# Kernel tuning notes

Measured on AMD Instinct MI355X. Metric: run time of the kernel, lower is better.

## Reference

```python
import jax, jax.numpy as jnp
import numpy as np

D_MODEL = 256
GAMMA = 0.9          # ret_D is built in the torch forward but never applied to the output; kept for fidelity notes
SCALE_BASE = 512     # XPOS default
TEMP = 10000.0
TWO_PI = 2.0 * np.pi


def sine_pos_embed(x):
    """DETR-style 1D sine position embedding with an all-ones mask (as in forward).
    x: [B,T,C] -> pos: [1,T,C] (mask is [1,T] ones, so batch dim broadcasts)."""
    T, C = x.shape[1], x.shape[2]
    x_embed = jnp.arange(1, T + 1, dtype=jnp.float32)          # cumsum of ones
    x_embed = x_embed / (x_embed[-1] + 1e-6) * TWO_PI          # normalize=True
    dim_t = TEMP ** (2.0 * (jnp.arange(C) // 2).astype(jnp.float32) / C)
    pos = x_embed[:, None] / dim_t                             # [T,C]
    pos = jnp.stack([jnp.sin(pos[:, 0::2]), jnp.cos(pos[:, 1::2])], axis=2).reshape(T, C)
    return pos[None].astype(x.dtype)


def _dup_interleave(m):
    # [L, d/2] -> [L, d], columns repeated pairwise: [a,b] -> [a,a,b,b]
    return jnp.repeat(m, 2, axis=-1)


def _rotate_every_two(x):
    x1, x2 = x[..., 0::2], x[..., 1::2]
    return jnp.stack([-x2, x1], axis=-1).reshape(x.shape)


def xpos_apply(x, downscale=False):
    """RetNet XPOS rotary embedding. x: [B,L,d]."""
    L, d = x.shape[1], x.shape[2]
    half = d // 2
    scale_vec = (jnp.arange(0, d, 2, dtype=jnp.float32) + 0.4 * d) / (1.4 * d)   # [d/2]
    power = jnp.arange(L, dtype=jnp.float32) / SCALE_BASE
    scale = scale_vec[None, :] ** power[:, None]                                  # [L, d/2]
    inv_freq = 1.0 / (TEMP ** (jnp.arange(half, dtype=jnp.float32) / half))
    sinusoid = jnp.arange(L, dtype=jnp.float32)[:, None] * inv_freq[None, :]      # [L, d/2]
    sin, cos = jnp.sin(sinusoid), jnp.cos(sinusoid)
    if downscale:
        scale = 1.0 / scale
    sin_s = _dup_interleave(sin * scale)[None].astype(x.dtype)   # [1,L,d]
    cos_s = _dup_interleave(cos * scale)[None].astype(x.dtype)
    return x * cos_s + _rotate_every_two(x) * sin_s


def setup_inputs() -> dict:
    key = jax.random.key(0)
    ks = jax.random.split(key, 8)
    B, TXT, VID, D = 16, 32, 2048, D_MODEL
    S = TXT + VID
    inp = {
        "src": jax.random.normal(ks[0], (B, S, D), dtype=jnp.float32),
        "learn_vid_ret": jax.random.normal(ks[1], (VID * VID, 1), dtype=jnp.float32),
        "W_txt_Q": jax.random.normal(ks[2], (D, D), dtype=jnp.float32) / D,
        "W_txt_K": jax.random.normal(ks[3], (D, D), dtype=jnp.float32) / D,
        "W_txt_V": jax.random.normal(ks[4], (D, D), dtype=jnp.float32) / D,
        "W_vid_Q": jax.random.normal(ks[5], (D, D), dtype=jnp.float32) / D,
        "W_vid_K": jax.random.normal(ks[6], (D, D), dtype=jnp.float32) / D,
        "W_vid_V": jax.random.normal(ks[7], (D, D), dtype=jnp.float32) / D,
        "txt_length": TXT,
    }
    return inp


def reference(src, learn_vid_ret, W_txt_Q, W_txt_K, W_txt_V, W_vid_Q, W_vid_K, W_vid_V, txt_length):
    S = src.shape[1]
    vid_length = S - txt_length

    # learned retention mask over the video block
    learn_ret = jax.nn.sigmoid(learn_vid_ret.reshape(vid_length, vid_length))
    diag = jnp.eye(vid_length, dtype=src.dtype)
    video_ret = (1.0 - diag) * learn_ret
    loss_sparsity = jnp.mean(jnp.abs(video_ret))

    # full [S,S] mask: ones everywhere, sigmoid(learned) on the vid-vid block
    ret_mask = jnp.ones((S, S), dtype=src.dtype).at[txt_length:, txt_length:].set(learn_ret)

    txt_mem = src[:, :txt_length]   # [B,TXT,D]
    vid_mem = src[:, txt_length:]   # [B,VID,D]

    pos = sine_pos_embed(txt_mem)   # [1,TXT,D]
    txt_Q = (pos + txt_mem) @ W_txt_Q
    txt_K = (pos + txt_mem) @ W_txt_K
    vid_Q = xpos_apply(vid_mem @ W_vid_Q)
    vid_K = xpos_apply(vid_mem @ W_vid_K, downscale=True)

    Q = jnp.concatenate([txt_Q, vid_Q], axis=1)                  # [B,S,D]
    K = jnp.concatenate([txt_K, vid_K], axis=1)                  # [B,S,D]
    V = jnp.concatenate([txt_mem @ W_txt_V, vid_mem @ W_vid_V], axis=1)

    # retention: QK^T elementwise-masked (no softmax), then weighted V sum
    scores = jnp.einsum('bsd,btd->bst', Q, K) * ret_mask[None]   # [B,S,S]
    out = scores @ V                                             # [B,S,D]
    return out, loss_sparsity
```

## Files before the change

kernel.cpp:

```cpp
#include <hip/hip_runtime.h>

#define B_   16
#define TXT  32
#define VID  2048
#define D_   256
#define S_   2080
#define SP   2176
#define NKT  34
#define ITERS 33

typedef unsigned short ushort_t;
typedef __attribute__((ext_vector_type(8))) short short8;
typedef __attribute__((ext_vector_type(4))) short short4v;
typedef __attribute__((ext_vector_type(4))) float f32x4;
typedef __attribute__((ext_vector_type(16))) float f32x16;

__device__ __forceinline__ ushort_t f2bf(float f) {
  unsigned u = __builtin_bit_cast(unsigned, f);
  unsigned r = (u + 0x7FFFu + ((u >> 16) & 1u)) >> 16;
  return (ushort_t)r;
}
__device__ __forceinline__ float bf2f(ushort_t h) {
  unsigned u = ((unsigned)h) << 16;
  return __builtin_bit_cast(float, u);
}

__device__ __forceinline__ void g2l16(void* lds, const void* g) {
  __builtin_amdgcn_global_load_lds(
      (const __attribute__((address_space(1))) char*)g,
      (__attribute__((address_space(3))) char*)lds, 16, 0, 0);
}

__device__ __forceinline__ f32x4 mfma16(short8 a, short8 b, f32x4 c) {
  return __builtin_amdgcn_mfma_f32_16x16x32_bf16(a, b, c, 0, 0, 0);
}
__device__ __forceinline__ f32x16 mfma32(short8 a, short8 b, f32x16 c) {
  return __builtin_amdgcn_mfma_f32_32x32x16_bf16(a, b, c, 0, 0, 0);
}


__global__ void tbl_kernel(float* __restrict__ tbl) {
  int idx = blockIdx.x * 256 + threadIdx.x;
  int n = idx >> 7, i = idx & 127;
  float invf = powf(10000.0f, -(float)i / 128.0f);
  float ang = (float)n * invf;
  float s, co;
  sincosf(ang, &s, &co);
  float sv = ((float)(2 * i) + 102.4f) / 358.4f;
  float sc = powf(sv, (float)n / 512.0f);
  float4 r;
  r.x = co * sc; r.y = s * sc; r.z = co / sc; r.w = s / sc;
  *(float4*)(tbl + (size_t)idx * 4) = r;
}

__global__ void sig_loss_kernel(const float* __restrict__ learn, ushort_t* __restrict__ sigp,
                                float* __restrict__ loss) {
  const int tid = threadIdx.x;
  const int base = (blockIdx.x * 256 + tid) * 8;
  float4 v0 = *(const float4*)(learn + base);
  float4 v1 = *(const float4*)(learn + base + 4);
  float vals[8] = {v0.x, v0.y, v0.z, v0.w, v1.x, v1.y, v1.z, v1.w};
  float acc = 0.f;
  short8 sh;
  #pragma unroll
  for (int j = 0; j < 8; ++j) {
    int idx = base + j;
    float s = 1.0f / (1.0f + expf(-vals[j]));
    sh[j] = (short)f2bf(s);
    int rr = idx >> 11, cc = idx & 2047;
    if (rr != cc) acc += s;
  }
  *(short8*)(sigp + base) = sh;
  __shared__ float red[256];
  red[tid] = acc;
  __syncthreads();
  #pragma unroll
  for (int st = 128; st > 0; st >>= 1) {
    if (tid < st) red[tid] += red[tid + st];
    __syncthreads();
  }
  if (tid == 0) atomicAdd(loss, red[0] * (1.0f / 4194304.0f));
}

__global__ void wt_kernel(const float* __restrict__ Wq, const float* __restrict__ Wk,
                          const float* __restrict__ Wv, ushort_t* __restrict__ WT) {
  __shared__ float t[64][68];
  const int k0 = blockIdx.x * 64, n0 = blockIdx.y * 64, mt = blockIdx.z;
  const float* W = (mt == 0) ? Wq : (mt == 1) ? Wk : Wv;
  int tid = threadIdx.x;
  int r = tid >> 4, cq = (tid & 15) * 4;
  #pragma unroll
  for (int m = 0; m < 4; ++m) {
    int k = m * 16 + r;
    float4 v = *(const float4*)(W + (size_t)(k0 + k) * 256 + n0 + cq);
    t[k][cq] = v.x; t[k][cq + 1] = v.y; t[k][cq + 2] = v.z; t[k][cq + 3] = v.w;
  }
  __syncthreads();
  #pragma unroll
  for (int m = 0; m < 4; ++m) {
    int n = m * 16 + r;
    short4v h;
    h[0] = (short)f2bf(t[cq + 0][n]);
    h[1] = (short)f2bf(t[cq + 1][n]);
    h[2] = (short)f2bf(t[cq + 2][n]);
    h[3] = (short)f2bf(t[cq + 3][n]);
    *(short4v*)(WT + ((size_t)mt * D_ + n0 + n) * D_ + k0 + cq) = h;
  }
}

__global__ void txt_kernel(const float* __restrict__ src,
                           const float* __restrict__ Wq, const float* __restrict__ Wk,
                           const float* __restrict__ Wv,
                           ushort_t* __restrict__ Qp, ushort_t* __restrict__ Ks,
                           ushort_t* __restrict__ VTs) {
  __shared__ float a_s[8][256];
  __shared__ float x_s[8][256];
  const int tg = blockIdx.x;
  const int b  = blockIdx.y;
  const int c  = threadIdx.x;
  #pragma unroll
  for (int t = 0; t < 8; ++t) {
    int row = tg * 8 + t;
    float x = src[((size_t)b * S_ + row) * D_ + c];
    float xe = (float)(row + 1) * (6.283185307179586f / (32.0f + 1e-6f));
    int i = c >> 1;
    float dimt = powf(10000.0f, (2.0f * (float)i) / 256.0f);
    float ang = xe / dimt;
    float pv = (c & 1) ? cosf(ang) : sinf(ang);
    x_s[t][c] = x;
    a_s[t][c] = x + pv;
  }
  __syncthreads();
  float q[8] = {0,0,0,0,0,0,0,0}, k[8] = {0,0,0,0,0,0,0,0}, v[8] = {0,0,0,0,0,0,0,0};
  for (int kk = 0; kk < 256; ++kk) {
    float wq = Wq[(size_t)kk * 256 + c];
    float wk = Wk[(size_t)kk * 256 + c];
    float wv = Wv[(size_t)kk * 256 + c];
    #pragma unroll
    for (int t = 0; t < 8; ++t) {
      q[t] = fmaf(a_s[t][kk], wq, q[t]);
      k[t] = fmaf(a_s[t][kk], wk, k[t]);
      v[t] = fmaf(x_s[t][kk], wv, v[t]);
    }
  }
  #pragma unroll
  for (int t = 0; t < 8; ++t) {
    int row = tg * 8 + t;
    Qp[((size_t)b * SP + row) * D_ + c] = f2bf(q[t]);
    Ks[(((size_t)(b * NKT)) << 14) + (c >> 4) * 1024 + row * 16 + (c & 15)] = f2bf(k[t]);
    VTs[(((size_t)(b * NKT)) << 14) + (row >> 4) * 4096 + c * 16 + (row & 15)] = f2bf(v[t]);
  }
}

__global__ __launch_bounds__(256, 2) void vid_gemm(
    const float* __restrict__ src, const ushort_t* __restrict__ WT,
    const float* __restrict__ tbl,
    ushort_t* __restrict__ Qp, ushort_t* __restrict__ Ks, ushort_t* __restrict__ VTs) {
  __shared__ __align__(16) ushort_t ldsA[64 * 64];
  __shared__ __align__(16) ushort_t ldsB[64 * 64];

  const int rt = blockIdx.x;
  const int b  = blockIdx.y;
  const int ct = blockIdx.z;
  const int nt = ct >> 2;
  const int n0 = (ct & 3) * 64;
  const int tid = threadIdx.x;
  const int wv = tid >> 6, lane = tid & 63, l15 = lane & 15, l4 = lane >> 4;

  f32x4 acc[4];
  #pragma unroll
  for (int t2 = 0; t2 < 4; ++t2) { acc[t2][0] = 0.f; acc[t2][1] = 0.f; acc[t2][2] = 0.f; acc[t2][3] = 0.f; }

  for (int kk = 0; kk < 256; kk += 64) {
    #pragma unroll
    for (int m = 0; m < 4; ++m) {
      int q = m * 256 + tid;
      int r = q >> 4;
      int kc = (q & 15) * 4;
      const float4 v = *(const float4*)(src + ((size_t)b * S_ + TXT + rt * 64 + r) * D_ + kk + kc);
      short4v h;
      h[0] = (short)f2bf(v.x); h[1] = (short)f2bf(v.y);
      h[2] = (short)f2bf(v.z); h[3] = (short)f2bf(v.w);
      int off = ((r << 7) + (kc << 1)) ^ ((r & 7) << 4);
      *(short4v*)((char*)ldsA + off) = h;
    }
    #pragma unroll
    for (int m = 0; m < 2; ++m) {
      int p = (m * 256 + tid) * 16;
      int nl = p >> 7;
      int c = (p & 127) ^ ((nl & 7) << 4);
      g2l16((char*)ldsB + p, (const char*)(WT + ((size_t)nt * D_ + n0 + nl) * D_ + kk) + c);
    }
    __syncthreads();
    #pragma unroll
    for (int ks = 0; ks < 2; ++ks) {
      int ar = wv * 16 + l15;
      int aoff = ((ar << 7) + ((ks * 32 + l4 * 8) << 1)) ^ ((ar & 7) << 4);
      short8 av = *(const short8*)((const char*)ldsA + aoff);
      #pragma unroll
      for (int t2 = 0; t2 < 4; ++t2) {
        int nl = t2 * 16 + l15;
        int boff = ((nl << 7) + ((ks * 32 + l4 * 8) << 1)) ^ ((nl & 7) << 4);
        short8 bv = *(const short8*)((const char*)ldsB + boff);
        acc[t2] = mfma16(av, bv, acc[t2]);
      }
    }
    __syncthreads();
  }

  const int rowl = wv * 16 + l4 * 4;
  if (nt < 2) {
    #pragma unroll
    for (int t2 = 0; t2 < 4; ++t2) {
      int c = n0 + t2 * 16 + l15;
      #pragma unroll
      for (int r = 0; r < 4; ++r) {
        int n = rt * 64 + rowl + r;
        float x = acc[t2][r];
        float xp = __shfl_xor(x, 1);
        const float4 tb = *(const float4*)(tbl + ((size_t)n * 128 + (c >> 1)) * 4);
        float cs = (nt == 0) ? tb.x : tb.z;
        float ss = (nt == 0) ? tb.y : tb.w;
        float val = (c & 1) ? fmaf(x, cs, xp * ss) : fmaf(x, cs, -xp * ss);
        if (nt == 0) {
          Qp[((size_t)b * SP + TXT + n) * D_ + c] = f2bf(val);
        } else {
          int kvg = TXT + n;
          Ks[(((size_t)(b * NKT + (kvg >> 6))) << 14) + (c >> 4) * 1024 + (kvg & 63) * 16 + (c & 15)] = f2bf(val);
        }
      }
    }
  } else {
    #pragma unroll
    for (int t2 = 0; t2 < 4; ++t2)
      #pragma unroll
      for (int r = 0; r < 4; ++r) {
        int rr = rowl + r;
        int cc = t2 * 16 + l15;
        int off = ((rr << 7) + (cc << 1)) ^ ((rr & 7) << 4);
        *(ushort_t*)((char*)ldsA + off) = f2bf(acc[t2][r]);
      }
    __syncthreads();
    int n = tid >> 2;
    int rc = (tid & 3) * 16;
    short8 o0, o1;
    #pragma unroll
    for (int j = 0; j < 8; ++j) {
      int rr = rc + j;
      int off = ((rr << 7) + (n << 1)) ^ ((rr & 7) << 4);
      o0[j] = *(const short*)((const char*)ldsA + off);
    }
    #pragma unroll
    for (int j = 0; j < 8; ++j) {
      int rr = rc + 8 + j;
      int off = ((rr << 7) + (n << 1)) ^ ((rr & 7) << 4);
      o1[j] = *(const short*)((const char*)ldsA + off);
    }
    int d = n0 + n;
    int kvg0 = TXT + rt * 64 + rc;
    size_t base = (((size_t)(b * NKT + (kvg0 >> 6))) << 14) + ((kvg0 >> 4) & 3) * 4096 + d * 16;
    *(short8*)(VTs + base) = o0;
    *(short8*)(VTs + base + 8) = o1;
  }
}

__global__ __launch_bounds__(256, 2) void attn_kernel(
    const ushort_t* __restrict__ Qp, const ushort_t* __restrict__ Ks,
    const ushort_t* __restrict__ VTs, const ushort_t* __restrict__ sigp,
    float* __restrict__ out) {
  __shared__ __align__(16) ushort_t Kb[16384];
  __shared__ __align__(16) ushort_t Vb[16384];
  __shared__ __align__(16) ushort_t Pb[4096];

  const int flat = blockIdx.x;
  const int wg = (flat & 7) * 66 + (flat >> 3);
  const int b  = wg / ITERS;
  const int qt = wg % ITERS;
  const int tid = threadIdx.x;
  const int wid = tid >> 6, lane = tid & 63;
  const int l31 = lane & 31, l5 = lane >> 5;
  const int qh = wid >> 1, kh = wid & 1, d0 = wid * 64;
  const int q0 = qt * 64;

  short8 qf[16];
  {
    const ushort_t* qrow = Qp + ((size_t)b * SP + q0 + qh * 32 + l31) * D_ + l5 * 8;
    #pragma unroll
    for (int ks = 0; ks < 16; ++ks) qf[ks] = *(const short8*)(qrow + ks * 16);
  }

  f32x16 oacc[2][2];
  #pragma unroll
  for (int i = 0; i < 2; ++i)
    #pragma unroll
    for (int j = 0; j < 2; ++j)
      #pragma unroll
      for (int r = 0; r < 16; ++r) oacc[i][j][r] = 0.f;

  const char* ksrc = (const char*)Ks + (((size_t)(b * NKT)) << 15);
  const char* vsrc = (const char*)VTs + (((size_t)(b * NKT)) << 15);

  ushort_t mvu[16];
  auto ldmask = [&](int t) {
    unsigned ki = (unsigned)(t * 64 + kh * 32 + l31 - TXT);
    bool kok = ki < (unsigned)VID;
    #pragma unroll
    for (int r = 0; r < 16; ++r) {
      int qloc = qh * 32 + (r & 3) + 8 * (r >> 2) + 4 * l5;
      unsigned qi = (unsigned)(q0 + qloc - TXT);
      bool ok = kok && (qi < (unsigned)VID);
      mvu[r] = sigp[ok ? ((size_t)qi * VID + ki) : 0];
    }
  };

  #pragma unroll
  for (int m = 0; m < 8; ++m) { int s = m * 256 + tid; g2l16((char*)Kb + s * 16, ksrc + s * 16); }
  __builtin_amdgcn_sched_barrier(0);
  ldmask(0);
  __builtin_amdgcn_sched_barrier(0);
  #pragma unroll
  for (int m = 0; m < 8; ++m) { int s = m * 256 + tid; g2l16((char*)Vb + s * 16, vsrc + s * 16); }
  __builtin_amdgcn_sched_barrier(0);
  asm volatile("s_waitcnt vmcnt(24)" ::: "memory");
  __builtin_amdgcn_sched_barrier(0);
  __builtin_amdgcn_s_barrier();
  __builtin_amdgcn_sched_barrier(0);

  for (int kt = 0; kt < ITERS; ++kt) {
    f32x16 s0, s1;
    #pragma unroll
    for (int r = 0; r < 16; ++r) { s0[r] = 0.f; s1[r] = 0.f; }
    const int krow = (kh * 32 + l31) * 32 + l5 * 16;
    __builtin_amdgcn_s_setprio(1);
    #pragma unroll
    for (int ks = 0; ks < 8; ++ks) {
      short8 kfa = *(const short8*)((const char*)Kb + ks * 2048 + krow);
      short8 kfb = *(const short8*)((const char*)Kb + (ks + 8) * 2048 + krow);
      s0 = mfma32(qf[ks], kfa, s0);
      s1 = mfma32(qf[ks + 8], kfb, s1);
    }
    __builtin_amdgcn_s_setprio(0);

    {
      unsigned ki = (unsigned)(kt * 64 + kh * 32 + l31 - TXT);
      bool kok = ki < (unsigned)VID;
      const int kvl = kh * 32 + l31;
      const int ksp = kvl >> 4;
      #pragma unroll
      for (int r = 0; r < 16; ++r) {
        int qloc = qh * 32 + (r & 3) + 8 * (r >> 2) + 4 * l5;
        unsigned qi = (unsigned)(q0 + qloc - TXT);
        float mvf = (kok && qi < (unsigned)VID) ? bf2f(mvu[r]) : 1.0f;
        float sv = (s0[r] + s1[r]) * mvf;
        int off = (ksp * 2048 + qloc * 32 + (kvl & 15) * 2)
                  ^ ((((unsigned)qloc >> 2) & 3) << 5) ^ ((ksp & 1) << 6);
        *(ushort_t*)((char*)Pb + off) = f2bf(sv);
      }
    }

    asm volatile("s_waitcnt vmcnt(0) lgkmcnt(0)" ::: "memory");
    __builtin_amdgcn_sched_barrier(0);
    __builtin_amdgcn_s_barrier();
    __builtin_amdgcn_sched_barrier(0);

    {
      const char* src = ksrc + ((size_t)(kt + 1) << 15);
      #pragma unroll
      for (int m = 0; m < 8; ++m) { int s = m * 256 + tid; g2l16((char*)Kb + s * 16, src + s * 16); }
    }
    __builtin_amdgcn_sched_barrier(0);

    __builtin_amdgcn_s_setprio(1);
    #pragma unroll
    for (int ks = 0; ks < 4; ++ks) {
      int p0 = (ks * 2048 + l31 * 32 + l5 * 16) ^ ((((unsigned)l31 >> 2) & 3) << 5) ^ ((ks & 1) << 6);
      int p1 = (ks * 2048 + (32 + l31) * 32 + l5 * 16) ^ ((((unsigned)(32 + l31) >> 2) & 3) << 5) ^ ((ks & 1) << 6);
      short8 pf0 = *(const short8*)((const char*)Pb + p0);
      short8 pf1 = *(const short8*)((const char*)Pb + p1);
      short8 vf0 = *(const short8*)((const char*)Vb + ks * 8192 + (d0 + l31) * 32 + l5 * 16);
      short8 vf1 = *(const short8*)((const char*)Vb + ks * 8192 + (d0 + 32 + l31) * 32 + l5 * 16);
      oacc[0][0] = mfma32(pf0, vf0, oacc[0][0]);
      oacc[0][1] = mfma32(pf0, vf1, oacc[0][1]);
      oacc[1][0] = mfma32(pf1, vf0, oacc[1][0]);
      oacc[1][1] = mfma32(pf1, vf1, oacc[1][1]);
    }
    __builtin_amdgcn_s_setprio(0);
    __builtin_amdgcn_sched_barrier(0);
    __builtin_amdgcn_s_barrier();
    __builtin_amdgcn_sched_barrier(0);

    ldmask(kt + 1);
    __builtin_amdgcn_sched_barrier(0);
    {
      const char* src = vsrc + ((size_t)(kt + 1) << 15);
      #pragma unroll
      for (int m = 0; m < 8; ++m) { int s = m * 256 + tid; g2l16((char*)Vb + s * 16, src + s * 16); }
    }
    __builtin_amdgcn_sched_barrier(0);
    asm volatile("s_waitcnt vmcnt(24)" ::: "memory");
    __builtin_amdgcn_sched_barrier(0);
    __builtin_amdgcn_s_barrier();
    __builtin_amdgcn_sched_barrier(0);
  }

  #pragma unroll
  for (int qg2 = 0; qg2 < 2; ++qg2)
    #pragma unroll
    for (int dg = 0; dg < 2; ++dg)
      #pragma unroll
      for (int reg = 0; reg < 16; ++reg) {
        int qg = q0 + qg2 * 32 + (reg & 3) + 8 * (reg >> 2) + 4 * l5;
        int dd = d0 + dg * 32 + l31;
        if (qg < S_) out[((size_t)b * S_ + qg) * D_ + dd] = oacc[qg2][dg][reg];
      }
}

extern "C" void kernel_launch(void* const* d_in, const int* in_sizes, int n_in,
                              void* d_out, int out_size, void* d_ws, size_t ws_size,
                              hipStream_t stream) {
  (void)in_sizes; (void)n_in; (void)out_size; (void)ws_size;
  const float* src   = (const float*)d_in[0];
  const float* learn = (const float*)d_in[1];
  const float* Wtq = (const float*)d_in[2];
  const float* Wtk = (const float*)d_in[3];
  const float* Wtv = (const float*)d_in[4];
  const float* Wvq = (const float*)d_in[5];
  const float* Wvk = (const float*)d_in[6];
  const float* Wvv = (const float*)d_in[7];
  float* out = (float*)d_out;

  char* ws = (char*)d_ws;
  const size_t QKV_ONE = (size_t)B_ * SP * D_ * 2;
  const size_t QP_OFF  = 0;
  const size_t KS_OFF  = QP_OFF + QKV_ONE;
  const size_t VT_OFF  = KS_OFF + QKV_ONE;
  const size_t SIG_OFF = VT_OFF + QKV_ONE;
  const size_t TBL_OFF = SIG_OFF + (size_t)VID * VID * 2;
  const size_t WT_OFF  = TBL_OFF + (size_t)VID * 128 * 4 * sizeof(float);

  ushort_t* Qp   = (ushort_t*)(ws + QP_OFF);
  ushort_t* Ks   = (ushort_t*)(ws + KS_OFF);
  ushort_t* VTs  = (ushort_t*)(ws + VT_OFF);
  ushort_t* sigp = (ushort_t*)(ws + SIG_OFF);
  float*    tbl  = (float*)(ws + TBL_OFF);
  ushort_t* WT   = (ushort_t*)(ws + WT_OFF);

  float* loss = out + (size_t)B_ * S_ * D_;

  hipMemsetAsync(ws, 0, SIG_OFF, stream);
  hipMemsetAsync(loss, 0, sizeof(float), stream);

  tbl_kernel<<<1024, 256, 0, stream>>>(tbl);
  sig_loss_kernel<<<2048, 256, 0, stream>>>(learn, sigp, loss);
  wt_kernel<<<dim3(4, 4, 3), 256, 0, stream>>>(Wvq, Wvk, Wvv, WT);
  txt_kernel<<<dim3(4, B_), 256, 0, stream>>>(src, Wtq, Wtk, Wtv, Qp, Ks, VTs);
  vid_gemm<<<dim3(32, B_, 12), 256, 0, stream>>>(src, WT, tbl, Qp, Ks, VTs);
  attn_kernel<<<dim3(528), 256, 0, stream>>>(Qp, Ks, VTs, sigp, out);
}
```

Measured before the change: 339.9 us.

## Stream-K attention over flattened tile space with atomic output accumulation

Flattens the (batch, q-tile, kv-tile) iteration space and splits it evenly across 512 persistent blocks. This replaces the 528 whole-row blocks, which quantize badly against the CU count. Partial outputs are flushed with float atomics into a zeroed output buffer, and Q is reloaded whenever the tile changes. The score MFMA is transposed so the mask is read from a transposed sigmoid table, and P is packed with v_cvt_pk_bf16 into a new swizzled layout. A dedicated kernel now zeroes only the pad regions instead of memsetting the whole workspace. The costs are atomic traffic, extra Q reloads at tile boundaries, and nondeterministic summation order.

```diff
diff --git a/kernel.cpp b/kernel.cpp
--- a/kernel.cpp
+++ b/kernel.cpp
@@ -7,7 +7,7 @@
 #define S_   2080
 #define SP   2176
 #define NKT  34
-#define ITERS 33
+#define GTOT 17424
 
 typedef unsigned short ushort_t;
 typedef __attribute__((ext_vector_type(8))) short short8;
@@ -53,25 +53,29 @@
   *(float4*)(tbl + (size_t)idx * 4) = r;
 }
 
-__global__ void sig_loss_kernel(const float* __restrict__ learn, ushort_t* __restrict__ sigp,
-                                float* __restrict__ loss) {
+__global__ void sig_kernel(const float* __restrict__ learn, ushort_t* __restrict__ sigT,
+                           float* __restrict__ loss) {
+  __shared__ ushort_t t[64][68];
+  __shared__ float red[256];
+  const int bi = blockIdx.x;
+  const int bj = blockIdx.y;
   const int tid = threadIdx.x;
-  const int base = (blockIdx.x * 256 + tid) * 8;
-  float4 v0 = *(const float4*)(learn + base);
-  float4 v1 = *(const float4*)(learn + base + 4);
-  float vals[8] = {v0.x, v0.y, v0.z, v0.w, v1.x, v1.y, v1.z, v1.w};
+  const int r = tid >> 2, c0 = (tid & 3) * 16;
+  const int q = bi * 64 + r;
   float acc = 0.f;
-  short8 sh;
-  #pragma unroll
-  for (int j = 0; j < 8; ++j) {
-    int idx = base + j;
-    float s = 1.0f / (1.0f + expf(-vals[j]));
-    sh[j] = (short)f2bf(s);
-    int rr = idx >> 11, cc = idx & 2047;
-    if (rr != cc) acc += s;
-  }
-  *(short8*)(sigp + base) = sh;
-  __shared__ float red[256];
+  const float* row = learn + (size_t)q * VID + bj * 64 + c0;
+  #pragma unroll
+  for (int j4 = 0; j4 < 4; ++j4) {
+    float4 v = *(const float4*)(row + j4 * 4);
+    float vv[4] = {v.x, v.y, v.z, v.w};
+    #pragma unroll
+    for (int j = 0; j < 4; ++j) {
+      int kv = bj * 64 + c0 + j4 * 4 + j;
+      float s = 1.0f / (1.0f + expf(-vv[j]));
+      if (q != kv) acc += s;
+      t[r][c0 + j4 * 4 + j] = f2bf(s);
+    }
+  }
   red[tid] = acc;
   __syncthreads();
   #pragma unroll
@@ -80,6 +84,34 @@
     __syncthreads();
   }
   if (tid == 0) atomicAdd(loss, red[0] * (1.0f / 4194304.0f));
+  short8 o0, o1;
+  #pragma unroll
+  for (int j = 0; j < 8; ++j) o0[j] = (short)t[c0 + j][r];
+  #pragma unroll
+  for (int j = 0; j < 8; ++j) o1[j] = (short)t[c0 + 8 + j][r];
+  ushort_t* dst = sigT + (size_t)(bj * 64 + r) * VID + bi * 64 + c0;
+  *(short8*)dst = o0;
+  *(short8*)(dst + 8) = o1;
+}
+
+__global__ void pad0_kernel(ushort_t* __restrict__ Qp, ushort_t* __restrict__ Ks,
+                            ushort_t* __restrict__ VTs) {
+  int i = blockIdx.x * 256 + threadIdx.x;
+  short8 z = {0, 0, 0, 0, 0, 0, 0, 0};
+  if (i < 49152) {
+    int bb = i / 3072, rem = i - bb * 3072;
+    int row = 2080 + (rem >> 5), c8 = (rem & 31) * 8;
+    *(short8*)(Qp + ((size_t)bb * SP + row) * D_ + c8) = z;
+  } else if (i < 65536) {
+    int j = i - 49152; int bb = j >> 10; int rem = j & 1023;
+    int kstep = rem >> 6, ch = rem & 63;
+    size_t base = ((size_t)(bb * NKT + 32)) << 14;
+    *(short8*)(Ks + base + kstep * 1024 + 512 + ch * 8) = z;
+  } else if (i < 81920) {
+    int j = i - 65536; int bb = j >> 10; int rem = j & 1023;
+    size_t base = (((size_t)(bb * NKT + 32)) << 14) + 8192;
+    *(short8*)(VTs + base + rem * 8) = z;
+  }
 }
 
 __global__ void wt_kernel(const float* __restrict__ Wq, const float* __restrict__ Wk,
@@ -266,28 +298,53 @@
 
 __global__ __launch_bounds__(256, 2) void attn_kernel(
     const ushort_t* __restrict__ Qp, const ushort_t* __restrict__ Ks,
-    const ushort_t* __restrict__ VTs, const ushort_t* __restrict__ sigp,
+    const ushort_t* __restrict__ VTs, const ushort_t* __restrict__ sigT,
     float* __restrict__ out) {
   __shared__ __align__(16) ushort_t Kb[16384];
   __shared__ __align__(16) ushort_t Vb[16384];
   __shared__ __align__(16) ushort_t Pb[4096];
 
-  const int flat = blockIdx.x;
-  const int wg = (flat & 7) * 66 + (flat >> 3);
-  const int b  = wg / ITERS;
-  const int qt = wg % ITERS;
+  const int kblk = blockIdx.x;
+  const int bs = (kblk & 7) * 64 + (kblk >> 3);
+  int g = bs * 34 + (bs >> 5);
+  const int gend = (bs + 1) * 34 + ((bs + 1) >> 5);
+
   const int tid = threadIdx.x;
   const int wid = tid >> 6, lane = tid & 63;
   const int l31 = lane & 31, l5 = lane >> 5;
   const int qh = wid >> 1, kh = wid & 1, d0 = wid * 64;
-  const int q0 = qt * 64;
+
+  int b = g / 1089, rem = g - b * 1089, qt = rem / 33, kvt = rem - qt * 33;
 
   short8 qf[16];
-  {
-    const ushort_t* qrow = Qp + ((size_t)b * SP + q0 + qh * 32 + l31) * D_ + l5 * 8;
+  auto ldq = [&](int bb, int qq) {
+    const ushort_t* qrow = Qp + ((size_t)bb * SP + qq * 64 + qh * 32 + l31) * D_ + l5 * 8;
     #pragma unroll
     for (int ks = 0; ks < 16; ++ks) qf[ks] = *(const short8*)(qrow + ks * 16);
-  }
+  };
+
+  ushort_t mvu[16];
+  auto ldmask = [&](int qq, int tt) {
+    unsigned qi = (unsigned)(qq * 64 + qh * 32 + l31 - TXT);
+    bool qok = qi < (unsigned)VID;
+    #pragma unroll
+    for (int r = 0; r < 16; ++r) {
+      unsigned ki = (unsigned)(tt * 64 + kh * 32 + (r & 3) + 8 * (r >> 2) + 4 * l5 - TXT);
+      bool ok = qok && (ki < (unsigned)VID);
+      mvu[r] = sigT[ok ? ((size_t)ki * VID + qi) : 0];
+    }
+  };
+
+  auto stageK = [&](int bb, int tt) {
+    const char* src = (const char*)Ks + (((size_t)(bb * NKT + tt)) << 15);
+    #pragma unroll
+    for (int m = 0; m < 8; ++m) { int s = m * 256 + tid; g2l16((char*)Kb + s * 16, src + s * 16); }
+  };
+  auto stageV = [&](int bb, int tt) {
+    const char* src = (const char*)VTs + (((size_t)(bb * NKT + tt)) << 15);
+    #pragma unroll
+    for (int m = 0; m < 8; ++m) { int s = m * 256 + tid; g2l16((char*)Vb + s * 16, src + s * 16); }
+  };
 
   f32x16 oacc[2][2];
   #pragma unroll
@@ -297,64 +354,67 @@
       #pragma unroll
       for (int r = 0; r < 16; ++r) oacc[i][j][r] = 0.f;
 
-  const char* ksrc = (const char*)Ks + (((size_t)(b * NKT)) << 15);
-  const char* vsrc = (const char*)VTs + (((size_t)(b * NKT)) << 15);
-
-  ushort_t mvu[16];
-  auto ldmask = [&](int t) {
-    unsigned ki = (unsigned)(t * 64 + kh * 32 + l31 - TXT);
-    bool kok = ki < (unsigned)VID;
-    #pragma unroll
-    for (int r = 0; r < 16; ++r) {
-      int qloc = qh * 32 + (r & 3) + 8 * (r >> 2) + 4 * l5;
-      unsigned qi = (unsigned)(q0 + qloc - TXT);
-      bool ok = kok && (qi < (unsigned)VID);
-      mvu[r] = sigp[ok ? ((size_t)qi * VID + ki) : 0];
-    }
+  auto flushO = [&](int bb, int qq) {
+    #pragma unroll
+    for (int qg2 = 0; qg2 < 2; ++qg2)
+      #pragma unroll
+      for (int dg = 0; dg < 2; ++dg)
+        #pragma unroll
+        for (int r = 0; r < 16; ++r) {
+          int qg = qq * 64 + qg2 * 32 + (r & 3) + 8 * (r >> 2) + 4 * l5;
+          int dd = d0 + dg * 32 + l31;
+          if (qg < S_)
+            unsafeAtomicAdd(&out[((size_t)bb * S_ + qg) * D_ + dd], oacc[qg2][dg][r]);
+          oacc[qg2][dg][r] = 0.f;
+        }
   };
 
-  #pragma unroll
-  for (int m = 0; m < 8; ++m) { int s = m * 256 + tid; g2l16((char*)Kb + s * 16, ksrc + s * 16); }
-  __builtin_amdgcn_sched_barrier(0);
-  ldmask(0);
-  __builtin_amdgcn_sched_barrier(0);
-  #pragma unroll
-  for (int m = 0; m < 8; ++m) { int s = m * 256 + tid; g2l16((char*)Vb + s * 16, vsrc + s * 16); }
-  __builtin_amdgcn_sched_barrier(0);
-  asm volatile("s_waitcnt vmcnt(24)" ::: "memory");
+  stageK(b, kvt);
+  ldmask(qt, kvt);
+  stageV(b, kvt);
+  ldq(b, qt);
+  asm volatile("s_waitcnt vmcnt(0)" ::: "memory");
   __builtin_amdgcn_sched_barrier(0);
   __builtin_amdgcn_s_barrier();
   __builtin_amdgcn_sched_barrier(0);
 
-  for (int kt = 0; kt < ITERS; ++kt) {
+  while (g < gend) {
+    int gn = (g + 1 < GTOT) ? g + 1 : GTOT - 1;
+    int nb = gn / 1089, nrem = gn - nb * 1089, nqt = nrem / 33, nkvt = nrem - nqt * 33;
+
     f32x16 s0, s1;
     #pragma unroll
     for (int r = 0; r < 16; ++r) { s0[r] = 0.f; s1[r] = 0.f; }
-    const int krow = (kh * 32 + l31) * 32 + l5 * 16;
+    const int arow = (kh * 32 + l31) * 32 + l5 * 16;
     __builtin_amdgcn_s_setprio(1);
     #pragma unroll
     for (int ks = 0; ks < 8; ++ks) {
-      short8 kfa = *(const short8*)((const char*)Kb + ks * 2048 + krow);
-      short8 kfb = *(const short8*)((const char*)Kb + (ks + 8) * 2048 + krow);
-      s0 = mfma32(qf[ks], kfa, s0);
-      s1 = mfma32(qf[ks + 8], kfb, s1);
+      short8 ka = *(const short8*)((const char*)Kb + ks * 2048 + arow);
+      short8 kc = *(const short8*)((const char*)Kb + (ks + 8) * 2048 + arow);
+      s0 = mfma32(ka, qf[ks], s0);
+      s1 = mfma32(kc, qf[ks + 8], s1);
     }
     __builtin_amdgcn_s_setprio(0);
 
     {
-      unsigned ki = (unsigned)(kt * 64 + kh * 32 + l31 - TXT);
-      bool kok = ki < (unsigned)VID;
-      const int kvl = kh * 32 + l31;
-      const int ksp = kvl >> 4;
+      unsigned qi = (unsigned)(qt * 64 + qh * 32 + l31 - TXT);
+      bool qok = qi < (unsigned)VID;
+      const int prow = qh * 32 + l31;
       #pragma unroll
-      for (int r = 0; r < 16; ++r) {
-        int qloc = qh * 32 + (r & 3) + 8 * (r >> 2) + 4 * l5;
-        unsigned qi = (unsigned)(q0 + qloc - TXT);
-        float mvf = (kok && qi < (unsigned)VID) ? bf2f(mvu[r]) : 1.0f;
-        float sv = (s0[r] + s1[r]) * mvf;
-        int off = (ksp * 2048 + qloc * 32 + (kvl & 15) * 2)
-                  ^ ((((unsigned)qloc >> 2) & 3) << 5) ^ ((ksp & 1) << 6);
-        *(ushort_t*)((char*)Pb + off) = f2bf(sv);
+      for (int t = 0; t < 4; ++t) {
+        float p[4];
+        #pragma unroll
+        for (int j = 0; j < 4; ++j) {
+          int r = t * 4 + j;
+          unsigned ki = (unsigned)(kvt * 64 + kh * 32 + j + 8 * t + 4 * l5 - TXT);
+          float mvf = (qok && ki < (unsigned)VID) ? bf2f(mvu[r]) : 1.0f;
+          p[j] = (s0[r] + s1[r]) * mvf;
+        }
+        unsigned w0, w1;
+        asm("v_cvt_pk_bf16_f32 %0, %1, %2" : "=v"(w0) : "v"(p[0]), "v"(p[1]));
+        asm("v_cvt_pk_bf16_f32 %0, %1, %2" : "=v"(w1) : "v"(p[2]), "v"(p[3]));
+        int off = (prow * 128 + kh * 64 + t * 16 + l5 * 8) ^ ((l31 & 7) << 4);
+        *(uint2*)((char*)Pb + off) = make_uint2(w0, w1);
       }
     }
 
@@ -363,18 +423,14 @@
     __builtin_amdgcn_s_barrier();
     __builtin_amdgcn_sched_barrier(0);
 
-    {
-      const char* src = ksrc + ((size_t)(kt + 1) << 15);
-      #pragma unroll
-      for (int m = 0; m < 8; ++m) { int s = m * 256 + tid; g2l16((char*)Kb + s * 16, src + s * 16); }
-    }
+    stageK(nb, nkvt);
     __builtin_amdgcn_sched_barrier(0);
 
     __builtin_amdgcn_s_setprio(1);
     #pragma unroll
     for (int ks = 0; ks < 4; ++ks) {
-      int p0 = (ks * 2048 + l31 * 32 + l5 * 16) ^ ((((unsigned)l31 >> 2) & 3) << 5) ^ ((ks & 1) << 6);
-      int p1 = (ks * 2048 + (32 + l31) * 32 + l5 * 16) ^ ((((unsigned)(32 + l31) >> 2) & 3) << 5) ^ ((ks & 1) << 6);
+      int p0 = (l31 * 128 + ks * 32 + l5 * 16) ^ ((l31 & 7) << 4);
+      int p1 = ((32 + l31) * 128 + ks * 32 + l5 * 16) ^ ((l31 & 7) << 4);
       short8 pf0 = *(const short8*)((const char*)Pb + p0);
       short8 pf1 = *(const short8*)((const char*)Pb + p1);
       short8 vf0 = *(const short8*)((const char*)Vb + ks * 8192 + (d0 + l31) * 32 + l5 * 16);
@@ -385,40 +441,35 @@
       oacc[1][1] = mfma32(pf1, vf1, oacc[1][1]);
     }
     __builtin_amdgcn_s_setprio(0);
+    asm volatile("s_waitcnt lgkmcnt(0)" ::: "memory");
     __builtin_amdgcn_sched_barrier(0);
     __builtin_amdgcn_s_barrier();
     __builtin_amdgcn_sched_barrier(0);
 
-    ldmask(kt + 1);
-    __builtin_amdgcn_sched_barrier(0);
-    {
-      const char* src = vsrc + ((size_t)(kt + 1) << 15);
-      #pragma unroll
-      for (int m = 0; m < 8; ++m) { int s = m * 256 + tid; g2l16((char*)Vb + s * 16, src + s * 16); }
-    }
+    ldmask(nqt, nkvt);
+    __builtin_amdgcn_sched_barrier(0);
+    if (nqt != qt || nb != b) {
+      flushO(b, qt);
+      ldq(nb, nqt);
+    }
+    __builtin_amdgcn_sched_barrier(0);
+    stageV(nb, nkvt);
     __builtin_amdgcn_sched_barrier(0);
     asm volatile("s_waitcnt vmcnt(24)" ::: "memory");
     __builtin_amdgcn_sched_barrier(0);
     __builtin_amdgcn_s_barrier();
     __builtin_amdgcn_sched_barrier(0);
-  }
-
-  #pragma unroll
-  for (int qg2 = 0; qg2 < 2; ++qg2)
-    #pragma unroll
-    for (int dg = 0; dg < 2; ++dg)
-      #pragma unroll
-      for (int reg = 0; reg < 16; ++reg) {
-        int qg = q0 + qg2 * 32 + (reg & 3) + 8 * (reg >> 2) + 4 * l5;
-        int dd = d0 + dg * 32 + l31;
-        if (qg < S_) out[((size_t)b * S_ + qg) * D_ + dd] = oacc[qg2][dg][reg];
-      }
+
+    b = nb; qt = nqt; kvt = nkvt; ++g;
+  }
+
+  flushO(b, qt);
 }
 
 extern "C" void kernel_launch(void* const* d_in, const int* in_sizes, int n_in,
                               void* d_out, int out_size, void* d_ws, size_t ws_size,
                               hipStream_t stream) {
-  (void)in_sizes; (void)n_in; (void)out_size; (void)ws_size;
+  (void)in_sizes; (void)n_in; (void)ws_size;
   const float* src   = (const float*)d_in[0];
   const float* learn = (const float*)d_in[1];
   const float* Wtq = (const float*)d_in[2];
@@ -441,19 +492,19 @@
   ushort_t* Qp   = (ushort_t*)(ws + QP_OFF);
   ushort_t* Ks   = (ushort_t*)(ws + KS_OFF);
   ushort_t* VTs  = (ushort_t*)(ws + VT_OFF);
-  ushort_t* sigp = (ushort_t*)(ws + SIG_OFF);
+  ushort_t* sigT = (ushort_t*)(ws + SIG_OFF);
   float*    tbl  = (float*)(ws + TBL_OFF);
   ushort_t* WT   = (ushort_t*)(ws + WT_OFF);
 
   float* loss = out + (size_t)B_ * S_ * D_;
-
-  hipMemsetAsync(ws, 0, SIG_OFF, stream);
-  hipMemsetAsync(loss, 0, sizeof(float), stream);
-
+  (void)loss;
+
+  hipMemsetAsync(d_out, 0, (size_t)out_size * sizeof(float), stream);
+  pad0_kernel<<<320, 256, 0, stream>>>(Qp, Ks, VTs);
   tbl_kernel<<<1024, 256, 0, stream>>>(tbl);
-  sig_loss_kernel<<<2048, 256, 0, stream>>>(learn, sigp, loss);
+  sig_kernel<<<dim3(32, 32), 256, 0, stream>>>(learn, sigT, out + (size_t)B_ * S_ * D_);
   wt_kernel<<<dim3(4, 4, 3), 256, 0, stream>>>(Wvq, Wvk, Wvv, WT);
   txt_kernel<<<dim3(4, B_), 256, 0, stream>>>(src, Wtq, Wtk, Wtv, Qp, Ks, VTs);
   vid_gemm<<<dim3(32, B_, 12), 256, 0, stream>>>(src, WT, tbl, Qp, Ks, VTs);
-  attn_kernel<<<dim3(528), 256, 0, stream>>>(Qp, Ks, VTs, sigp, out);
-}
+  attn_kernel<<<dim3(512), 256, 0, stream>>>(Qp, Ks, VTs, sigT, out);
+}
```

After: 298.1 us. -12.3%, faster.
